# Performance work log

Hardware: AMD Instinct MI355X
Metric: run time of the kernel (lower is better)

The kernel has to match this reference:

```python
import jax, jax.numpy as jnp
import numpy as np


def setup_inputs() -> dict:
    key = jax.random.key(0)
    k1, k2, k3 = jax.random.split(key, 3)
    N, P, D = 4, 1024, 1024
    E, H = 8, 2048
    sequences = jax.random.normal(k1, (N, P, D), dtype=jnp.float32)
    # torch Linear layout: weight [out, in]
    gate_W = jax.random.normal(k2, (E, D), dtype=jnp.float32) * (1.0 / np.sqrt(D))
    gate_b = jnp.zeros((E,), dtype=jnp.float32)
    # xavier_uniform bound for Linear(D, H)
    bound = float(np.sqrt(6.0 / (D + H)))
    expert_W = jax.random.uniform(k3, (E, H, D), dtype=jnp.float32, minval=-bound, maxval=bound)
    expert_b = jnp.zeros((E, H), dtype=jnp.float32)
    return {"sequences": sequences, "gate_W": gate_W, "gate_b": gate_b,
            "expert_W": expert_W, "expert_b": expert_b, "moe_top_k": 2}


def reference(sequences, gate_W, gate_b, expert_W, expert_b, moe_top_k):
    N, P, D = sequences.shape
    E = expert_W.shape[0]
    x = sequences.reshape(-1, D)                       # [T, D]
    gating_scores = jax.nn.softmax(x @ gate_W.T + gate_b, axis=-1)  # [T, E]
    _, top_k_idx = jax.lax.top_k(gating_scores, moe_top_k)          # [T, k]
    # boolean dispatch mask: token t routed to expert e (topk indices are unique)
    mask = jax.nn.one_hot(top_k_idx, E, dtype=x.dtype).sum(axis=1)  # [T, E] in {0,1}
    out = jnp.zeros((x.shape[0], expert_W.shape[1]), dtype=x.dtype)
    # loop over small fixed expert set; masked dense GEMM per expert
    for e in range(E):
        out = out + mask[:, e:e + 1] * (x @ expert_W[e].T + expert_b[e])
    # NOTE: original adds UNWEIGHTED expert outputs, then divides by top_k
    out = out / moe_top_k
    gating_variances = jnp.var(gating_scores, axis=0, ddof=1)  # torch.var unbiased
    return out.reshape(N, P, -1), gating_variances
```

## Files before the change

kernel.cpp:

```cpp
#include <hip/hip_runtime.h>


#define NTOK 4096
#define DIM  1024
#define NEXP 8
#define HID  2048

#define BM 128
#define BN 128
#define BK 64

using u16    = unsigned short;
using u16x4  = __attribute__((ext_vector_type(4))) unsigned short;
using u16x8  = __attribute__((ext_vector_type(8))) unsigned short;
using bf16x8 = __attribute__((ext_vector_type(8))) __bf16;
using f32x4  = __attribute__((ext_vector_type(4))) float;

typedef const __attribute__((address_space(1))) unsigned char* gas1p;
typedef __attribute__((address_space(3))) unsigned char* gas3p;

__device__ __forceinline__ void gload16(void* lds, const void* g) {
  __builtin_amdgcn_global_load_lds((gas1p)g, (gas3p)lds, 16, 0, 0);
}

__device__ inline u16 f2bf(float f) {
  union { float f; unsigned u; } v; v.f = f;
  unsigned r = v.u + 0x7fffu + ((v.u >> 16) & 1u);
  return (u16)(r >> 16);
}
__device__ inline float bf2f(u16 b) {
  union { unsigned u; float f; } v; v.u = ((unsigned)b) << 16; return v.f;
}

__global__ __launch_bounds__(256) void convert_bf16(
    const float* __restrict__ in, u16* __restrict__ out) {
  int i = blockIdx.x * 256 + threadIdx.x;
  const float4* p = (const float4*)in + (size_t)i * 2;
  float4 a = p[0], b = p[1];
  u16x8 r;
  r[0] = f2bf(a.x); r[1] = f2bf(a.y); r[2] = f2bf(a.z); r[3] = f2bf(a.w);
  r[4] = f2bf(b.x); r[5] = f2bf(b.y); r[6] = f2bf(b.z); r[7] = f2bf(b.w);
  *((u16x8*)out + i) = r;
}

__global__ __launch_bounds__(256) void gate_kernel(
    const float* __restrict__ x, const float* __restrict__ gW,
    const float* __restrict__ gb, float* __restrict__ probs,
    int* __restrict__ top2, u16* __restrict__ xbf) {
  const int wave = threadIdx.x >> 6;
  const int lane = threadIdx.x & 63;
  const int t = blockIdx.x * 4 + wave;

  const float4* xrow = (const float4*)(x + (size_t)t * DIM);
  double acc[NEXP];
#pragma unroll
  for (int e = 0; e < NEXP; ++e) acc[e] = 0.0;

#pragma unroll
  for (int c = 0; c < 4; ++c) {
    int idx = c * 64 + lane;
    float4 xv = xrow[idx];
    u16x4 bv;
    bv[0] = f2bf(xv.x); bv[1] = f2bf(xv.y); bv[2] = f2bf(xv.z); bv[3] = f2bf(xv.w);
    *(u16x4*)(xbf + (size_t)t * DIM + 4 * idx) = bv;
#pragma unroll
    for (int e = 0; e < NEXP; ++e) {
      float4 wv = ((const float4*)(gW + (size_t)e * DIM))[idx];
      acc[e] += (double)xv.x * wv.x + (double)xv.y * wv.y +
                (double)xv.z * wv.z + (double)xv.w * wv.w;
    }
  }
#pragma unroll
  for (int e = 0; e < NEXP; ++e) {
    double v = acc[e];
#pragma unroll
    for (int off = 32; off > 0; off >>= 1) v += __shfl_down(v, off);
    acc[e] = v;
  }

  if (lane == 0) {
    double logits[NEXP];
#pragma unroll
    for (int e = 0; e < NEXP; ++e) logits[e] = acc[e] + (double)gb[e];
    double m = logits[0];
#pragma unroll
    for (int e = 1; e < NEXP; ++e) m = fmax(m, logits[e]);
    double p[NEXP], s = 0.0;
#pragma unroll
    for (int e = 0; e < NEXP; ++e) { p[e] = exp(logits[e] - m); s += p[e]; }
#pragma unroll
    for (int e = 0; e < NEXP; ++e) p[e] /= s;

    int i1 = 0;
#pragma unroll
    for (int e = 1; e < NEXP; ++e) if (p[e] > p[i1]) i1 = e;
    int i2 = (i1 == 0) ? 1 : 0;
#pragma unroll
    for (int e = 0; e < NEXP; ++e) {
      if (e != i1 && p[e] > p[i2]) i2 = e;
    }

#pragma unroll
    for (int e = 0; e < NEXP; ++e) probs[(size_t)t * NEXP + e] = (float)p[e];
    top2[t] = i1 | (i2 << 4);
  }
}

__global__ __launch_bounds__(256) void route_kernel(
    const float* __restrict__ probs, const int* __restrict__ top2,
    int* __restrict__ counts, int* __restrict__ lists,
    float* __restrict__ var_out) {
  const int e = blockIdx.x;
  const int tid = threadIdx.x;
  const int lane = tid & 63;
  const int wave = tid >> 6;

  __shared__ int wsum[4];
  __shared__ double ds[4], dq[4];

  double s = 0.0, q = 0.0;
  int base = 0;

  for (int c = 0; c < NTOK / 256; ++c) {
    int t = c * 256 + tid;
    float p = probs[(size_t)t * NEXP + e];
    s += (double)p;
    q += (double)p * (double)p;

    int m = top2[t];
    bool f = ((m & 15) == e) || (((m >> 4) & 15) == e);
    unsigned long long bal = __ballot(f);
    int before = __popcll(bal & ((1ull << lane) - 1ull));
    if (lane == 0) wsum[wave] = __popcll(bal);
    __syncthreads();
    int woff = 0;
#pragma unroll
    for (int w = 0; w < 4; ++w) if (w < wave) woff += wsum[w];
    int ctotal = wsum[0] + wsum[1] + wsum[2] + wsum[3];
    if (f) lists[e * NTOK + base + woff + before] = t;
    base += ctotal;
    __syncthreads();
  }
  if (tid == 0) counts[e] = base;

#pragma unroll
  for (int off = 32; off > 0; off >>= 1) {
    s += __shfl_down(s, off);
    q += __shfl_down(q, off);
  }
  if (lane == 0) { ds[wave] = s; dq[wave] = q; }
  __syncthreads();
  if (tid == 0) {
    double S = ds[0] + ds[1] + ds[2] + ds[3];
    double Q = dq[0] + dq[1] + dq[2] + dq[3];
    var_out[e] = (float)((Q - S * S / (double)NTOK) / (double)(NTOK - 1));
  }
}

__global__ __launch_bounds__(256, 2) void expert_gemm(
    const u16* __restrict__ xbf, const u16* __restrict__ wbf,
    const int* __restrict__ counts, const int* __restrict__ lists,
    const int* __restrict__ top2, u16* __restrict__ pbf) {
  __shared__ u16 As[BM * BK];
  __shared__ u16 Bs[BN * BK];
  __shared__ int tok[BM];
  __shared__ int kslot[BM];

  const int hw = blockIdx.x;
  const int L  = (hw & 7) * 512 + (hw >> 3);
  const int cb = L >> 8;
  const int e  = (L >> 5) & 7;
  const int rb = L & 31;
  const int cnt = counts[e];
  if (rb * BM >= cnt) return;

  const int tid  = threadIdx.x;
  const int wave = tid >> 6;
  const int lane = tid & 63;

  if (tid < BM) {
    int gi = rb * BM + tid;
    int tr = (gi < cnt) ? lists[e * NTOK + gi] : -1;
    tok[tid] = tr;
    kslot[tid] = (tr >= 0 && (top2[tr] & 15) == e) ? 0 : 1;
  }
  __syncthreads();

  const u16* asrc[4];
  const u16* bsrc[4];
  int ldsoff[4];
#pragma unroll
  for (int j = 0; j < 4; ++j) {
    const int idx  = (j * 4 + wave) * 64 + lane;
    const int row  = idx >> 3;
    const int c16  = (idx & 7) ^ (row & 7);
    int tr = tok[row]; if (tr < 0) tr = 0;
    asrc[j] = xbf + (size_t)tr * DIM + c16 * 8;
    bsrc[j] = wbf + ((size_t)e * HID + (size_t)cb * BN + row) * DIM + c16 * 8;
    ldsoff[j] = (j * 4 + wave) * 512;
  }

  const int wm = (wave >> 1) * 64;
  const int wn = (wave & 1) * 64;
  const int lr = lane & 15;
  const int hk = lane >> 4;

  f32x4 acc[4][4];
#pragma unroll
  for (int m = 0; m < 4; ++m)
#pragma unroll
    for (int n = 0; n < 4; ++n) acc[m][n] = (f32x4)(0.0f);

  for (int k0 = 0; k0 < DIM; k0 += BK) {
#pragma unroll
    for (int j = 0; j < 4; ++j) gload16(&As[ldsoff[j]], asrc[j] + k0);
#pragma unroll
    for (int j = 0; j < 4; ++j) gload16(&Bs[ldsoff[j]], bsrc[j] + k0);

    __syncthreads();

    bf16x8 fa[2][4], fb[2][4];
#pragma unroll
    for (int kk = 0; kk < 2; ++kk) {
#pragma unroll
      for (int m = 0; m < 4; ++m) {
        const int row = wm + m * 16 + lr;
        const int c16 = (kk * 4 + hk) ^ (row & 7);
        fa[kk][m] = *(const bf16x8*)&As[row * 64 + c16 * 8];
      }
#pragma unroll
      for (int n = 0; n < 4; ++n) {
        const int row = wn + n * 16 + lr;
        const int c16 = (kk * 4 + hk) ^ (row & 7);
        fb[kk][n] = *(const bf16x8*)&Bs[row * 64 + c16 * 8];
      }
    }

#pragma unroll
    for (int kk = 0; kk < 2; ++kk)
#pragma unroll
      for (int m = 0; m < 4; ++m)
#pragma unroll
        for (int n = 0; n < 4; ++n)
          acc[m][n] = __builtin_amdgcn_mfma_f32_16x16x32_bf16(
              fa[kk][m], fb[kk][n], acc[m][n], 0, 0, 0);

    __syncthreads();
  }

#pragma unroll
  for (int n = 0; n < 4; ++n) {
    const int hcol = cb * BN + wn + n * 16 + lr;
#pragma unroll
    for (int m = 0; m < 4; ++m) {
#pragma unroll
      for (int i = 0; i < 4; ++i) {
        int rloc = wm + m * 16 + hk * 4 + i;
        int tr = tok[rloc];
        if (tr >= 0)
          pbf[((size_t)kslot[rloc] * NTOK + tr) * HID + hcol] =
              f2bf(acc[m][n][i]);
      }
    }
  }
}

__global__ __launch_bounds__(256) void combine_kernel(
    const u16* __restrict__ pbf, const int* __restrict__ top2,
    const float* __restrict__ eb, float* __restrict__ out) {
  const int t = blockIdx.x;
  const int h = threadIdx.x * 8;
  const int m2 = top2[t];
  const int e1 = m2 & 15, e2 = (m2 >> 4) & 15;

  u16x8 p0 = *(const u16x8*)&pbf[(size_t)t * HID + h];
  u16x8 p1 = *(const u16x8*)&pbf[((size_t)NTOK + t) * HID + h];
  const float4* b1 = (const float4*)&eb[e1 * HID + h];
  const float4* b2 = (const float4*)&eb[e2 * HID + h];
  float4 b1a = b1[0], b1b = b1[1], b2a = b2[0], b2b = b2[1];

  float4 o0, o1;
  o0.x = 0.5f * (bf2f(p0[0]) + bf2f(p1[0]) + b1a.x + b2a.x);
  o0.y = 0.5f * (bf2f(p0[1]) + bf2f(p1[1]) + b1a.y + b2a.y);
  o0.z = 0.5f * (bf2f(p0[2]) + bf2f(p1[2]) + b1a.z + b2a.z);
  o0.w = 0.5f * (bf2f(p0[3]) + bf2f(p1[3]) + b1a.w + b2a.w);
  o1.x = 0.5f * (bf2f(p0[4]) + bf2f(p1[4]) + b1b.x + b2b.x);
  o1.y = 0.5f * (bf2f(p0[5]) + bf2f(p1[5]) + b1b.y + b2b.y);
  o1.z = 0.5f * (bf2f(p0[6]) + bf2f(p1[6]) + b1b.z + b2b.z);
  o1.w = 0.5f * (bf2f(p0[7]) + bf2f(p1[7]) + b1b.w + b2b.w);

  float4* po = (float4*)&out[(size_t)t * HID + h];
  po[0] = o0; po[1] = o1;
}

extern "C" void kernel_launch(void* const* d_in, const int* in_sizes, int n_in,
                              void* d_out, int out_size, void* d_ws, size_t ws_size,
                              hipStream_t stream) {
  const float* x  = (const float*)d_in[0];
  const float* gW = (const float*)d_in[1];
  const float* gb = (const float*)d_in[2];
  const float* eW = (const float*)d_in[3];
  const float* eb = (const float*)d_in[4];

  float* out = (float*)d_out;
  float* var_out = out + (size_t)NTOK * HID;

  char* ws = (char*)d_ws;
  int*   counts = (int*)ws;
  int*   lists  = (int*)(ws + 1024);
  float* probs  = (float*)(ws + 1024 + 131072);
  int*   top2   = (int*)(ws + 1024 + 2 * 131072);
  u16*   xbf    = (u16*)(ws + 294912);
  u16*   wbf    = (u16*)((char*)xbf + (size_t)NTOK * DIM * 2);
  u16*   pbf    = (u16*)((char*)wbf + (size_t)NEXP * HID * DIM * 2);

  convert_bf16<<<(NEXP * HID * DIM) / (256 * 8), 256, 0, stream>>>(eW, wbf);
  gate_kernel<<<NTOK / 4, 256, 0, stream>>>(x, gW, gb, probs, top2, xbf);
  route_kernel<<<NEXP, 256, 0, stream>>>(probs, top2, counts, lists, var_out);
  expert_gemm<<<NEXP * (NTOK / BM) * (HID / BN), 256, 0, stream>>>(
      xbf, wbf, counts, lists, top2, pbf);
  combine_kernel<<<NTOK, 256, 0, stream>>>(pbf, top2, eb, out);
}
```

Baseline: 111.1 us.

## Merge weight conversion with gating and compact expert GEMM tile grid

Folds the expert-weight bf16 conversion and the gating kernel into one launch, removing a kernel boundary. The expert GEMM grid shrinks from the full E×32×16 set of tiles to a fixed compact count, and each block finds its expert and row/column tile from a prefix walk over the per-expert token counts. This avoids launching mostly-empty blocks that exit at once. Launch bounds are raised to allow four blocks per CU. MAXTILES=1152 assumes the total routed tiles never exceed that bound, and the higher occupancy target may force register spills.

```diff
diff --git a/kernel.cpp b/kernel.cpp
--- a/kernel.cpp
+++ b/kernel.cpp
@@ -9,6 +9,9 @@
 #define BM 128
 #define BN 128
 #define BK 64
+
+#define CONV_BLOCKS 8192
+#define MAXTILES 1152
 
 using u16    = unsigned short;
 using u16x4  = __attribute__((ext_vector_type(4))) unsigned short;
@@ -32,24 +35,25 @@
   union { unsigned u; float f; } v; v.u = ((unsigned)b) << 16; return v.f;
 }
 
-__global__ __launch_bounds__(256) void convert_bf16(
-    const float* __restrict__ in, u16* __restrict__ out) {
-  int i = blockIdx.x * 256 + threadIdx.x;
-  const float4* p = (const float4*)in + (size_t)i * 2;
-  float4 a = p[0], b = p[1];
-  u16x8 r;
-  r[0] = f2bf(a.x); r[1] = f2bf(a.y); r[2] = f2bf(a.z); r[3] = f2bf(a.w);
-  r[4] = f2bf(b.x); r[5] = f2bf(b.y); r[6] = f2bf(b.z); r[7] = f2bf(b.w);
-  *((u16x8*)out + i) = r;
-}
-
-__global__ __launch_bounds__(256) void gate_kernel(
+__global__ __launch_bounds__(256) void pre_kernel(
+    const float* __restrict__ eW, u16* __restrict__ wbf,
     const float* __restrict__ x, const float* __restrict__ gW,
     const float* __restrict__ gb, float* __restrict__ probs,
     int* __restrict__ top2, u16* __restrict__ xbf) {
+  if (blockIdx.x < CONV_BLOCKS) {
+    int i = blockIdx.x * 256 + threadIdx.x;
+    const float4* p = (const float4*)eW + (size_t)i * 2;
+    float4 a = p[0], b = p[1];
+    u16x8 r;
+    r[0] = f2bf(a.x); r[1] = f2bf(a.y); r[2] = f2bf(a.z); r[3] = f2bf(a.w);
+    r[4] = f2bf(b.x); r[5] = f2bf(b.y); r[6] = f2bf(b.z); r[7] = f2bf(b.w);
+    *((u16x8*)wbf + i) = r;
+    return;
+  }
+
   const int wave = threadIdx.x >> 6;
   const int lane = threadIdx.x & 63;
-  const int t = blockIdx.x * 4 + wave;
+  const int t = (blockIdx.x - CONV_BLOCKS) * 4 + wave;
 
   const float4* xrow = (const float4*)(x + (size_t)t * DIM);
   double acc[NEXP];
@@ -157,7 +161,7 @@
   }
 }
 
-__global__ __launch_bounds__(256, 2) void expert_gemm(
+__global__ __launch_bounds__(256, 4) void expert_gemm(
     const u16* __restrict__ xbf, const u16* __restrict__ wbf,
     const int* __restrict__ counts, const int* __restrict__ lists,
     const int* __restrict__ top2, u16* __restrict__ pbf) {
@@ -166,13 +170,21 @@
   __shared__ int tok[BM];
   __shared__ int kslot[BM];
 
-  const int hw = blockIdx.x;
-  const int L  = (hw & 7) * 512 + (hw >> 3);
-  const int cb = L >> 8;
-  const int e  = (L >> 5) & 7;
-  const int rb = L & 31;
-  const int cnt = counts[e];
-  if (rb * BM >= cnt) return;
+  int rem = blockIdx.x;
+  int e = 0, cnt = 0;
+#pragma unroll
+  for (int ee = 0; ee < NEXP; ++ee) {
+    int c = counts[ee];
+    int nt = ((c + BM - 1) >> 7) << 4;
+    if (e == ee) {
+      if (rem < nt) { cnt = c; }
+      else { rem -= nt; e = ee + 1; }
+    }
+  }
+  if (e >= NEXP) return;
+  cnt = counts[e];
+  const int rb = rem >> 4;
+  const int cb = rem & 15;
 
   const int tid  = threadIdx.x;
   const int wave = tid >> 6;
@@ -314,10 +326,10 @@
   u16*   wbf    = (u16*)((char*)xbf + (size_t)NTOK * DIM * 2);
   u16*   pbf    = (u16*)((char*)wbf + (size_t)NEXP * HID * DIM * 2);
 
-  convert_bf16<<<(NEXP * HID * DIM) / (256 * 8), 256, 0, stream>>>(eW, wbf);
-  gate_kernel<<<NTOK / 4, 256, 0, stream>>>(x, gW, gb, probs, top2, xbf);
+  pre_kernel<<<CONV_BLOCKS + NTOK / 4, 256, 0, stream>>>(
+      eW, wbf, x, gW, gb, probs, top2, xbf);
   route_kernel<<<NEXP, 256, 0, stream>>>(probs, top2, counts, lists, var_out);
-  expert_gemm<<<NEXP * (NTOK / BM) * (HID / BN), 256, 0, stream>>>(
+  expert_gemm<<<MAXTILES, 256, 0, stream>>>(
       xbf, wbf, counts, lists, top2, pbf);
   combine_kernel<<<NTOK, 256, 0, stream>>>(pbf, top2, eb, out);
 }
```

Result: slower. 139.0 us (+25.1%).
